# Kernel optimization log

Hardware: AMD Instinct MI355X
Metric: run time of the kernel (lower is better)

Reference implementation:

```python
import jax, jax.numpy as jnp
import numpy as np

LN_EPS = 1e-5


def setup_inputs() -> dict:
    key = jax.random.key(0)
    ks = jax.random.split(key, 10)
    B, T, S, C = 8, 1024, 2048, 1024
    sd = 1.0 / np.sqrt(C)
    return {
        "x": jax.random.normal(ks[0], (B, T, C), jnp.float32),
        "lfb_feats": jax.random.normal(ks[1], (B, S, C), jnp.float32),
        "theta_w": jax.random.normal(ks[2], (C, C), jnp.float32) * sd,
        "theta_b": jax.random.normal(ks[3], (C,), jnp.float32) * 0.01,
        "phi_w": jax.random.normal(ks[4], (C, C), jnp.float32) * sd,
        "phi_b": jax.random.normal(ks[5], (C,), jnp.float32) * 0.01,
        "gi_w": jax.random.normal(ks[6], (C, C), jnp.float32) * sd,
        "gi_b": jax.random.normal(ks[7], (C,), jnp.float32) * 0.01,
        "ln_g": jnp.ones((C,), jnp.float32),
        "ln_b": jnp.zeros((C,), jnp.float32),
        "fc_w": jax.random.normal(ks[8], (C, C), jnp.float32) * sd,
        "fc_b": jax.random.normal(ks[9], (C,), jnp.float32) * 0.01,
    }


def _layernorm(h, g, b):
    mu = jnp.mean(h, axis=-1, keepdims=True)
    var = jnp.var(h, axis=-1, keepdims=True)
    return (h - mu) * jax.lax.rsqrt(var + LN_EPS) * g + b


def reference(x, lfb_feats, theta_w, theta_b, phi_w, phi_b, gi_w, gi_b,
              ln_g, ln_b, fc_w, fc_b):
    # x: [B,T,C], lfb_feats: [B,S,C]. 1x1 Conv1d == per-token linear on channels.
    C = x.shape[-1]
    scale = jnp.sqrt(jnp.asarray(C, x.dtype))  # NOTE: 1/sqrt(1/C) = sqrt(C) (as in source)
    theta = jnp.einsum('btc,oc->bto', x, theta_w) + theta_b          # [B,T,C]
    phi = jnp.einsum('bsc,oc->bso', lfb_feats, phi_w) + phi_b        # [B,S,C]
    gi = jnp.einsum('bsc,oc->bso', lfb_feats, gi_w) + gi_b           # [B,S,C]
    attn = jax.nn.softmax(jnp.einsum('btc,bsc->bts', theta, phi) * scale, axis=-1)
    out = jnp.einsum('bts,bsc->btc', attn, gi)                       # [B,T,C]
    out = jax.nn.relu(_layernorm(out, ln_g, ln_b))
    out = jnp.einsum('btc,oc->bto', out, fc_w) + fc_b                # fc (dropout = identity at eval)
    return out + x                                                   # residual, [B,T,C]
```

## Files before the change

### kernel.cpp

```cpp
#include <hip/hip_runtime.h>


#define BM 128
#define BN 128
#define BK 64

typedef __attribute__((ext_vector_type(8))) short short8;
typedef __attribute__((ext_vector_type(4))) float f32x4;
typedef __attribute__((ext_vector_type(4))) unsigned short us4;

enum { MODE_SPLIT = 0, MODE_TRANS = 1, MODE_F32 = 2, MODE_FINAL = 3 };

__device__ __forceinline__ float b2f(unsigned short u) {
  union { unsigned int i; float f; } x;
  x.i = ((unsigned int)u) << 16;
  return x.f;
}
__device__ __forceinline__ unsigned short f2b(float f) {
  unsigned int u = __float_as_uint(f);
  unsigned int r = (u + 0x7FFFu + ((u >> 16) & 1u)) >> 16;
  return (unsigned short)r;
}

__device__ __forceinline__ void async_cp16(const unsigned short* g,
                                           unsigned short* l) {
  __builtin_amdgcn_global_load_lds(
      (const __attribute__((address_space(1))) void*)g,
      (__attribute__((address_space(3))) void*)l, 16, 0, 0);
}

__global__ __launch_bounds__(256) void split_xlfb(
    const float* __restrict__ lfb, const float* __restrict__ x,
    const float* __restrict__ g, unsigned short* __restrict__ ls,
    unsigned short* __restrict__ xs, float* __restrict__ v, int Ms) {
  const int id = blockIdx.x;
  const int t = threadIdx.x;
  const int c = t * 4;
  if (id < Ms) {
    __shared__ float red[4];
    f32x4 xv = *(const f32x4*)&lfb[(size_t)id * 1024 + c];
    f32x4 gg = *(const f32x4*)&g[c];
    us4 hi, lo;
    float s = 0.f;
#pragma unroll
    for (int i = 0; i < 4; ++i) {
      hi[i] = f2b(xv[i]);
      lo[i] = f2b(xv[i] - b2f(hi[i]));
      s += xv[i] * gg[i];
    }
    *(us4*)&ls[(size_t)id * 2048 + c] = hi;
    *(us4*)&ls[(size_t)id * 2048 + 1024 + c] = lo;
    for (int o = 32; o; o >>= 1) s += __shfl_xor(s, o, 64);
    if ((t & 63) == 0) red[t >> 6] = s;
    __syncthreads();
    if (t == 0) v[id] = red[0] + red[1] + red[2] + red[3];
  } else {
    const int r = id - Ms;
    f32x4 xv = *(const f32x4*)&x[(size_t)r * 1024 + c];
    us4 hi, lo;
#pragma unroll
    for (int i = 0; i < 4; ++i) {
      hi[i] = f2b(xv[i]);
      lo[i] = f2b(xv[i] - b2f(hi[i]));
    }
    *(us4*)&xs[(size_t)r * 2048 + c] = hi;
    *(us4*)&xs[(size_t)r * 2048 + 1024 + c] = lo;
  }
}

__global__ __launch_bounds__(256) void cvt2_bf16(const float* __restrict__ s0,
                                                 unsigned short* __restrict__ d0,
                                                 const float* __restrict__ s1,
                                                 unsigned short* __restrict__ d1) {
  int b = blockIdx.x;
  const float* src = (b < 1024) ? s0 : s1;
  unsigned short* dst = (b < 1024) ? d0 : d1;
  int g = (b & 1023) * 256 + threadIdx.x;
  f32x4 v = *(const f32x4*)&src[g * 4];
  us4 o;
#pragma unroll
  for (int i = 0; i < 4; ++i) o[i] = f2b(v[i]);
  *(us4*)&dst[(size_t)g * 4] = o;
}

__global__ __launch_bounds__(256) void transpose_split2(
    const float* __restrict__ W0, unsigned short* __restrict__ T0,
    const float* __restrict__ W1, unsigned short* __restrict__ T1) {
  __shared__ float tile[64][65];
  const int sel = blockIdx.y >> 4;
  const float* W = sel ? W1 : W0;
  unsigned short* T = sel ? T1 : T0;
  const int bo = (blockIdx.y & 15) * 64;
  const int bc = blockIdx.x * 64;
  const int t = threadIdx.x;
  const int tr = t >> 4;
  const int tc = (t & 15) * 4;
#pragma unroll
  for (int i = 0; i < 4; ++i) {
    f32x4 v = *(const f32x4*)&W[(size_t)(bo + tr + 16 * i) * 1024 + bc + tc];
#pragma unroll
    for (int j = 0; j < 4; ++j) tile[tr + 16 * i][tc + j] = v[j];
  }
  __syncthreads();
#pragma unroll
  for (int i = 0; i < 4; ++i) {
    const int c = bc + tr + 16 * i;
    us4 hi, lo;
#pragma unroll
    for (int j = 0; j < 4; ++j) {
      float v = tile[tc + j][tr + 16 * i];
      hi[j] = f2b(v);
      lo[j] = f2b(v - b2f(hi[j]));
    }
    *(us4*)&T[(size_t)c * 2048 + bo + tc] = hi;
    *(us4*)&T[(size_t)c * 2048 + 1024 + bo + tc] = lo;
  }
}

__global__ __launch_bounds__(256) void make_g(
    const unsigned short* __restrict__ tB, const float* __restrict__ bth,
    float* __restrict__ g) {
  const int d = blockIdx.x * 4 + (threadIdx.x >> 6);
  const int lane = threadIdx.x & 63;
  float s = 0.f;
#pragma unroll
  for (int i = 0; i < 4; ++i) {
    const int o0 = lane * 4 + i * 256;
    us4 h = *(const us4*)&tB[(size_t)d * 2048 + o0];
    us4 lo = *(const us4*)&tB[(size_t)d * 2048 + 1024 + o0];
    f32x4 bb = *(const f32x4*)&bth[o0];
#pragma unroll
    for (int j = 0; j < 4; ++j) s += (b2f(h[j]) + b2f(lo[j])) * bb[j];
  }
  for (int o = 32; o; o >>= 1) s += __shfl_xor(s, o, 64);
  if (lane == 0) g[d] = s;
}

__global__ __launch_bounds__(256) void reduce_g(const float* __restrict__ P,
                                                unsigned short* __restrict__ Gs) {
  const int d = blockIdx.x;
  const int c = threadIdx.x * 4;
  f32x4 s = *(const f32x4*)&P[(size_t)d * 1024 + c];
#pragma unroll
  for (int z = 1; z < 8; ++z) {
    f32x4 p = *(const f32x4*)&P[(size_t)z * 1048576 + (size_t)d * 1024 + c];
#pragma unroll
    for (int i = 0; i < 4; ++i) s[i] += p[i];
  }
  us4 hi, lo;
#pragma unroll
  for (int i = 0; i < 4; ++i) {
    hi[i] = f2b(s[i]);
    lo[i] = f2b(s[i] - b2f(hi[i]));
  }
  *(us4*)&Gs[(size_t)d * 2048 + c] = hi;
  *(us4*)&Gs[(size_t)d * 2048 + 1024 + c] = lo;
}

template <int MODE>
__global__ __launch_bounds__(256, 4) void gemm_bt(
    const unsigned short* __restrict__ A, const unsigned short* __restrict__ B,
    void* __restrict__ Cout, const float* __restrict__ bias,
    const float* __restrict__ resid, int M, int N, int K, int lda, int ldb,
    int ldc, long long sA, long long sB, long long sC, long long sBias,
    int awrap, int awoff, int bwrap, int bwoff, int NBk, int MBk, int mbx,
    int swz, int kzoff) {
  __shared__ __align__(16) unsigned short As[BM * BK];
  __shared__ __align__(16) unsigned short Bs[BN * BK];

  const int tid = threadIdx.x;
  const int l = tid & 63;
  const int w = tid >> 6;
  const int wm = w >> 1, wn = w & 1;
  const int ln = l & 15, lq = l >> 4;

  int bmi, bni, bzi;
  {
    const int id = blockIdx.x;
    if (swz == 1) {
      bzi = id & 7;
      const int r = id >> 3;
      bmi = r % mbx;
      bni = r / mbx;
    } else if (swz == 2) {
      bzi = 0;
      const int r = id >> 3;
      bmi = (id & 7) * mbx + r % mbx;
      bni = r / mbx;
    } else {
      bni = id % NBk;
      const int rem = id / NBk;
      bmi = rem % MBk;
      bzi = rem / MBk;
    }
  }
  const int bm = bmi * BM;
  const int bn = bni * BN;
  const unsigned short* Ab = A + (size_t)bzi * (size_t)sA;
  const unsigned short* Bb = B + (size_t)bzi * (size_t)sB;
  const float* bz = bias ? bias + (size_t)bzi * (size_t)sBias : nullptr;
  const int kbase = bzi * kzoff;

  const int arow = tid >> 3;
  const int acol = (((tid & 7) ^ ((tid >> 3) & 7)) * 8);
  const int ldsbase = (tid & 0xC0) * 8;

  f32x4 acc[4][4];
#pragma unroll
  for (int i = 0; i < 4; ++i)
#pragma unroll
    for (int j = 0; j < 4; ++j) acc[i][j] = (f32x4){0.f, 0.f, 0.f, 0.f};

  const int sw = ln & 7;

  for (int k0 = 0; k0 < K; k0 += BK) {
    const int kg = k0 + kbase;
    const int ka = (kg < awrap) ? kg : kg - awoff;
    const int kb = (kg < bwrap) ? kg : kg - bwoff;
#pragma unroll
    for (int it = 0; it < 4; ++it) {
      const int r = it * 32 + arow;
      async_cp16(Ab + (size_t)(bm + r) * lda + ka + acol,
                 &As[it * 2048 + ldsbase]);
    }
#pragma unroll
    for (int it = 0; it < 4; ++it) {
      const int r = it * 32 + arow;
      async_cp16(Bb + (size_t)(bn + r) * ldb + kb + acol,
                 &Bs[it * 2048 + ldsbase]);
    }
    __syncthreads();

#pragma unroll
    for (int ks = 0; ks < 2; ++ks) {
      short8 a[4], b[4];
      const int kof = ((ks * 4 + lq) ^ sw) * 8;
#pragma unroll
      for (int i = 0; i < 4; ++i)
        a[i] = *(const short8*)&As[(wm * 64 + i * 16 + ln) * BK + kof];
#pragma unroll
      for (int j = 0; j < 4; ++j)
        b[j] = *(const short8*)&Bs[(wn * 64 + j * 16 + ln) * BK + kof];
#pragma unroll
      for (int i = 0; i < 4; ++i)
#pragma unroll
        for (int j = 0; j < 4; ++j)
          acc[i][j] = __builtin_amdgcn_mfma_f32_16x16x32_bf16(a[i], b[j],
                                                              acc[i][j], 0, 0, 0);
    }
    __syncthreads();
  }

  float* Cf = (float*)Cout + (size_t)bzi * (size_t)sC;
  unsigned short* Cb = (unsigned short*)Cout + (size_t)bzi * (size_t)sC;

  if constexpr (MODE == MODE_TRANS) {
#pragma unroll
    for (int i = 0; i < 4; ++i) {
      const int gm0 = bm + wm * 64 + i * 16 + lq * 4;
      const int bt = gm0 >> 11;
      const int sr = gm0 & 2047;
#pragma unroll
      for (int j = 0; j < 4; ++j) {
        const int gn = bn + wn * 64 + j * 16 + ln;
        const float bv2 = (bz != nullptr) ? bz[gn] : 0.f;
        us4 o;
#pragma unroll
        for (int r = 0; r < 4; ++r) o[r] = f2b(acc[i][j][r] + bv2);
        *(us4*)&Cb[(size_t)bt * 2097152 + (size_t)gn * 2048 + sr] = o;
      }
    }
  } else {
#pragma unroll
    for (int j = 0; j < 4; ++j) {
      const int gn = bn + wn * 64 + j * 16 + ln;
      const float bv2 = (bz != nullptr) ? bz[gn] : 0.f;
#pragma unroll
      for (int i = 0; i < 4; ++i) {
        const int gm0 = bm + wm * 64 + i * 16 + lq * 4;
#pragma unroll
        for (int r = 0; r < 4; ++r) {
          const int gm = gm0 + r;
          const float v = acc[i][j][r] + bv2;
          if constexpr (MODE == MODE_SPLIT) {
            unsigned short hi = f2b(v);
            Cb[(size_t)gm * ldc + gn] = hi;
            Cb[(size_t)gm * ldc + gn + (ldc >> 1)] = f2b(v - b2f(hi));
          } else if constexpr (MODE == MODE_F32) {
            Cf[(size_t)gm * ldc + gn] = v;
          } else if constexpr (MODE == MODE_FINAL) {
            const size_t idx = (size_t)gm * ldc + gn;
            Cf[idx] = v + resid[idx];
          }
        }
      }
    }
  }
}

__global__ __launch_bounds__(256) void softmax_rows(
    const float* __restrict__ logit, unsigned short* __restrict__ attn) {
  const int row = blockIdx.x;
  const float* L = logit + (size_t)row * 2048;
  unsigned short* O = attn + (size_t)row * 2048;
  const int t = threadIdx.x;
  __shared__ float red[8];

  f32x4 v0 = *(const f32x4*)&L[t * 4];
  f32x4 v1 = *(const f32x4*)&L[t * 4 + 1024];
  float m = fmaxf(fmaxf(fmaxf(v0[0], v0[1]), fmaxf(v0[2], v0[3])),
                  fmaxf(fmaxf(v1[0], v1[1]), fmaxf(v1[2], v1[3])));
  for (int o = 32; o; o >>= 1) m = fmaxf(m, __shfl_xor(m, o, 64));
  if ((t & 63) == 0) red[t >> 6] = m;
  __syncthreads();
  m = fmaxf(fmaxf(red[0], red[1]), fmaxf(red[2], red[3]));

  float e[8];
  float s = 0.f;
#pragma unroll
  for (int i = 0; i < 4; ++i) { e[i] = __expf(32.f * (v0[i] - m)); s += e[i]; }
#pragma unroll
  for (int i = 0; i < 4; ++i) { e[4 + i] = __expf(32.f * (v1[i] - m)); s += e[4 + i]; }
  for (int o = 32; o; o >>= 1) s += __shfl_xor(s, o, 64);
  if ((t & 63) == 0) red[4 + (t >> 6)] = s;
  __syncthreads();
  s = red[4] + red[5] + red[6] + red[7];
  const float inv = 1.f / s;
  us4 o0, o1;
#pragma unroll
  for (int i = 0; i < 4; ++i) { o0[i] = f2b(e[i] * inv); o1[i] = f2b(e[4 + i] * inv); }
  *(us4*)&O[t * 4] = o0;
  *(us4*)&O[t * 4 + 1024] = o1;
}

__global__ __launch_bounds__(256) void ln_relu(
    const float* __restrict__ X, const float* __restrict__ g,
    const float* __restrict__ b, unsigned short* __restrict__ H) {
  const int row = blockIdx.x;
  const float* x = X + (size_t)row * 1024;
  unsigned short* h = H + (size_t)row * 1024;
  const int t = threadIdx.x;
  __shared__ float red[8];
  f32x4 v = *(const f32x4*)&x[t * 4];
  float s = v[0] + v[1] + v[2] + v[3];
  float q = v[0] * v[0] + v[1] * v[1] + v[2] * v[2] + v[3] * v[3];
  for (int o = 32; o; o >>= 1) {
    s += __shfl_xor(s, o, 64);
    q += __shfl_xor(q, o, 64);
  }
  if ((t & 63) == 0) { red[t >> 6] = s; red[4 + (t >> 6)] = q; }
  __syncthreads();
  s = red[0] + red[1] + red[2] + red[3];
  q = red[4] + red[5] + red[6] + red[7];
  const float mean = s * (1.f / 1024.f);
  const float var = q * (1.f / 1024.f) - mean * mean;
  const float rstd = rsqrtf(var + 1e-5f);
  us4 o;
#pragma unroll
  for (int i = 0; i < 4; ++i) {
    const int c = t * 4 + i;
    const float y = (v[i] - mean) * rstd * g[c] + b[c];
    o[i] = f2b(fmaxf(y, 0.f));
  }
  *(us4*)&h[t * 4] = o;
}

extern "C" void kernel_launch(void* const* d_in, const int* in_sizes, int n_in,
                              void* d_out, int out_size, void* d_ws,
                              size_t ws_size, hipStream_t stream) {
  const float* x = (const float*)d_in[0];
  const float* lfb = (const float*)d_in[1];
  const float* th_w = (const float*)d_in[2];
  const float* th_b = (const float*)d_in[3];
  const float* ph_w = (const float*)d_in[4];
  const float* gi_w = (const float*)d_in[6];
  const float* gi_b = (const float*)d_in[7];
  const float* lng = (const float*)d_in[8];
  const float* lnb = (const float*)d_in[9];
  const float* fc_w = (const float*)d_in[10];
  const float* fc_b = (const float*)d_in[11];
  float* outf = (float*)d_out;
  char* ws = (char*)d_ws;

  const size_t MB = 1048576;
  int nb = 1;
  for (int cand = 8; cand >= 1; cand >>= 1)
    if ((size_t)cand * 24 * MB + 18 * MB <= ws_size) { nb = cand; break; }

  char* tail = ws + (size_t)nb * 24 * MB;
  unsigned short* tA = (unsigned short*)(tail);
  unsigned short* tB = (unsigned short*)(tail + 4 * MB);
  unsigned short* Gs = (unsigned short*)(tail + 8 * MB);
  unsigned short* giw = (unsigned short*)(tail + 12 * MB);
  unsigned short* fcw = (unsigned short*)(tail + 14 * MB);
  float* gv = (float*)(tail + 16 * MB);
  float* vb = (float*)(tail + 16 * MB + 65536);

  dim3 blk(256);
  transpose_split2<<<dim3(16, 32), blk, 0, stream>>>(th_w, tA, ph_w, tB);
  make_g<<<dim3(256), blk, 0, stream>>>(tB, th_b, gv);
  if (nb >= 2) {
    float* gpart = (float*)ws;
    gemm_bt<MODE_F32><<<dim3(512), blk, 0, stream>>>(
        tB, tA, gpart, nullptr, nullptr, 1024, 1024, 384, 2048, 2048, 1024,
        0, 0, 1048576LL, 0, 2048, 2048, 1024, 1024, 8, 8, 8, 1, 384);
    reduce_g<<<dim3(1024), blk, 0, stream>>>(gpart, Gs);
  } else {
    gemm_bt<MODE_SPLIT><<<dim3(64), blk, 0, stream>>>(
        tB, tA, Gs, nullptr, nullptr, 1024, 1024, 3072, 2048, 2048, 2048,
        0, 0, 0, 0, 2048, 2048, 1024, 1024, 8, 8, 1, 2, 0);
  }
  cvt2_bf16<<<dim3(2048), blk, 0, stream>>>(gi_w, giw, fc_w, fcw);

  for (int b0 = 0; b0 < 8; b0 += nb) {
    unsigned short* xs = (unsigned short*)(ws);
    float* logit = (float*)(ws);
    unsigned short* ls = (unsigned short*)(ws + (size_t)nb * 8 * MB);
    unsigned short* ys = (unsigned short*)(ws + (size_t)nb * 16 * MB);
    unsigned short* giT = (unsigned short*)(ws + (size_t)nb * 20 * MB);
    unsigned short* attn = ys;
    float* outp = (float*)ws;
    unsigned short* h = giT;

    const float* xb = x + (size_t)b0 * 1048576;
    const float* lfbb = lfb + (size_t)b0 * 2097152;
    float* ob = outf + (size_t)b0 * 1048576;
    const int Ms = nb * 2048;
    const int Mt = nb * 1024;
    const int zswz = (nb == 8) ? 1 : 0;

    split_xlfb<<<dim3(Ms + Mt), blk, 0, stream>>>(lfbb, xb, gv, ls, xs, vb, Ms);
    gemm_bt<MODE_TRANS><<<dim3(8 * (Ms / 128)), blk, 0, stream>>>(
        ls, giw, giT, gi_b, nullptr, Ms, 1024, 1024, 2048, 1024, 2048,
        0, 0, 0, 0, 1024, 0, 1024, 0, 8, Ms / 128, Ms / 1024, 2, 0);
    gemm_bt<MODE_SPLIT><<<dim3(8 * (Mt / 128)), blk, 0, stream>>>(
        xs, Gs, ys, nullptr, nullptr, Mt, 1024, 3072, 2048, 2048, 2048,
        0, 0, 0, 0, 2048, 2048, 1024, 1024, 8, Mt / 128, Mt / 1024, 2, 0);
    gemm_bt<MODE_F32><<<dim3(16 * 8 * nb), blk, 0, stream>>>(
        ys, ls, logit, vb, nullptr, 1024, 2048, 3072, 2048, 2048, 2048,
        2097152LL, 4194304LL, 2097152LL, 2048LL, 2048, 2048, 1024, 1024,
        16, 8, 8, zswz, 0);
    softmax_rows<<<dim3(Mt), blk, 0, stream>>>(logit, attn);
    gemm_bt<MODE_F32><<<dim3(8 * 8 * nb), blk, 0, stream>>>(
        attn, giT, outp, nullptr, nullptr, 1024, 1024, 2048, 2048, 2048, 1024,
        2097152LL, 2097152LL, 1048576LL, 0, 2048, 0, 2048, 0, 8, 8, 8, zswz, 0);
    ln_relu<<<dim3(Mt), blk, 0, stream>>>(outp, lng, lnb, h);
    gemm_bt<MODE_FINAL><<<dim3(8 * (Mt / 128)), blk, 0, stream>>>(
        h, fcw, ob, fc_b, xb, Mt, 1024, 1024, 1024, 1024, 1024,
        0, 0, 0, 0, 1024, 0, 1024, 0, 8, Mt / 128, Mt / 1024, 2, 0);
  }
}
```

Measured before the change: 514.2 us.

## Add 256x256-tile 8-wave GEMM kernel for gi projection and logits GEMMs

Result: faster. 501.3 us (-2.5%).

```diff
diff --git a/kernel.cpp b/kernel.cpp
--- a/kernel.cpp
+++ b/kernel.cpp
@@ -298,6 +298,203 @@
   }
 }
 
+__device__ __forceinline__ void ld8f(const unsigned short* Lb, int roff, int ln,
+                                     int lq, int sw, short8* a) {
+#pragma unroll
+  for (int mi = 0; mi < 4; ++mi)
+#pragma unroll
+    for (int ks = 0; ks < 2; ++ks)
+      a[mi * 2 + ks] = *(const short8*)&Lb[(roff + mi * 16 + ln) * 64 +
+                                           (((ks * 4 + lq) ^ sw) * 8)];
+}
+__device__ __forceinline__ void ld4f(const unsigned short* Lb, int roff, int ln,
+                                     int lq, int sw, short8* b) {
+#pragma unroll
+  for (int ni = 0; ni < 2; ++ni)
+#pragma unroll
+    for (int ks = 0; ks < 2; ++ks)
+      b[ni * 2 + ks] = *(const short8*)&Lb[(roff + ni * 16 + ln) * 64 +
+                                           (((ks * 4 + lq) ^ sw) * 8)];
+}
+template <int MH, int NH>
+__device__ __forceinline__ void mfmaQ(f32x4 (&acc)[8][4], const short8* a,
+                                      const short8* b) {
+  __builtin_amdgcn_s_setprio(1);
+#pragma unroll
+  for (int mi = 0; mi < 4; ++mi)
+#pragma unroll
+    for (int ni = 0; ni < 2; ++ni)
+#pragma unroll
+      for (int ks = 0; ks < 2; ++ks)
+        acc[MH * 4 + mi][NH * 2 + ni] = __builtin_amdgcn_mfma_f32_16x16x32_bf16(
+            a[mi * 2 + ks], b[ni * 2 + ks], acc[MH * 4 + mi][NH * 2 + ni], 0, 0,
+            0);
+  __builtin_amdgcn_s_setprio(0);
+}
+
+template <int MODE>
+__global__ __launch_bounds__(512, 1) void gemm8(
+    const unsigned short* __restrict__ A, const unsigned short* __restrict__ B,
+    void* __restrict__ Cout, const float* __restrict__ bias, int M, int N,
+    int K, int lda, int ldb, int ldc, long long sA, long long sB, long long sC,
+    long long sBias, int awrap, int awoff, int bwrap, int bwoff, int NBk,
+    int MBk, int mbx, int swz) {
+  __shared__ __align__(16) unsigned short lds[2][4][8192];
+
+  const int tid = threadIdx.x;
+  const int l = tid & 63;
+  const int w = tid >> 6;
+  const int wm = w >> 2;
+  const int wn = w & 3;
+  const int ln = l & 15, lq = l >> 4;
+  const int sw = ln & 7;
+
+  int bmi, bni, bzi;
+  {
+    const int id = blockIdx.x;
+    if (swz == 1) {
+      bzi = id & 7;
+      const int r = id >> 3;
+      bmi = r % mbx;
+      bni = r / mbx;
+    } else if (swz == 2) {
+      bzi = 0;
+      const int r = id >> 3;
+      bmi = (id & 7) * mbx + r % mbx;
+      bni = r / mbx;
+    } else {
+      bni = id % NBk;
+      const int rem = id / NBk;
+      bmi = rem % MBk;
+      bzi = rem / MBk;
+    }
+  }
+  const int bm = bmi * 256;
+  const int bn = bni * 256;
+  const unsigned short* Ab = A + (size_t)bzi * (size_t)sA;
+  const unsigned short* Bb = B + (size_t)bzi * (size_t)sB;
+  const float* bz = bias ? bias + (size_t)bzi * (size_t)sBias : nullptr;
+
+  const int srow = tid >> 3;
+  const int schk = ((tid & 7) ^ ((tid >> 3) & 7)) * 8;
+  const int sdst0 = (tid & 448) * 8;
+
+  auto stageA = [&](int d, int half, int kk) {
+#pragma unroll
+    for (int j = 0; j < 2; ++j)
+      async_cp16(Ab + (size_t)(bm + half * 128 + srow + j * 64) * lda + kk +
+                     schk,
+                 &lds[d][half][sdst0 + j * 4096]);
+  };
+  auto stageB = [&](int d, int half, int kk) {
+#pragma unroll
+    for (int j = 0; j < 2; ++j)
+      async_cp16(Bb + (size_t)(bn + half * 128 + srow + j * 64) * ldb + kk +
+                     schk,
+                 &lds[d][2 + half][sdst0 + j * 4096]);
+  };
+  auto wrapA = [&](int kg) { return (kg < awrap) ? kg : kg - awoff; };
+  auto wrapB = [&](int kg) { return (kg < bwrap) ? kg : kg - bwoff; };
+
+  f32x4 acc[8][4];
+#pragma unroll
+  for (int i = 0; i < 8; ++i)
+#pragma unroll
+    for (int j = 0; j < 4; ++j) acc[i][j] = (f32x4){0.f, 0.f, 0.f, 0.f};
+
+  const int nt = K >> 6;
+
+  stageA(0, 0, wrapA(0));
+  stageA(0, 1, wrapA(0));
+  stageB(0, 0, wrapB(0));
+  stageB(0, 1, wrapB(0));
+  if (nt > 1) {
+    stageB(1, 0, wrapB(64));
+    stageB(1, 1, wrapB(64));
+    asm volatile("s_waitcnt vmcnt(4)" : : : "memory");
+  } else {
+    asm volatile("s_waitcnt vmcnt(0)" : : : "memory");
+  }
+  __builtin_amdgcn_s_barrier();
+
+  const unsigned short* LA;
+  const unsigned short* LB;
+  short8 a0[8], a1[8], b0[4], b1[4];
+  const int broff = (wn & 1) * 64;
+  const int bslot = 2 + (wn >> 1);
+
+  for (int t = 0; t < nt; ++t) {
+    const int d = t & 1;
+    LA = &lds[d][wm][0];
+    LB = &lds[d][bslot][0];
+    ld8f(LA, 0, ln, lq, sw, a0);
+    ld4f(LB, broff, ln, lq, sw, b0);
+    if (t + 1 < nt) stageA(d ^ 1, 0, wrapA((t + 1) * 64));
+    __builtin_amdgcn_s_barrier();
+    asm volatile("s_waitcnt lgkmcnt(0)" : : : "memory");
+    __builtin_amdgcn_sched_barrier(0);
+    mfmaQ<0, 0>(acc, a0, b0);
+    __builtin_amdgcn_s_barrier();
+    ld4f(LB, broff + 32, ln, lq, sw, b1);
+    if (t + 1 < nt) stageA(d ^ 1, 1, wrapA((t + 1) * 64));
+    __builtin_amdgcn_s_barrier();
+    asm volatile("s_waitcnt lgkmcnt(0)" : : : "memory");
+    __builtin_amdgcn_sched_barrier(0);
+    mfmaQ<0, 1>(acc, a0, b1);
+    __builtin_amdgcn_s_barrier();
+    ld8f(LA, 64, ln, lq, sw, a1);
+    if (t + 2 < nt) stageB(d, 0, wrapB((t + 2) * 64));
+    __builtin_amdgcn_s_barrier();
+    asm volatile("s_waitcnt lgkmcnt(0)" : : : "memory");
+    __builtin_amdgcn_sched_barrier(0);
+    mfmaQ<1, 1>(acc, a1, b1);
+    __builtin_amdgcn_s_barrier();
+    if (t + 2 < nt) stageB(d, 1, wrapB((t + 2) * 64));
+    __builtin_amdgcn_s_barrier();
+    mfmaQ<1, 0>(acc, a1, b0);
+    if (t + 2 < nt) {
+      asm volatile("s_waitcnt vmcnt(4)" : : : "memory");
+    } else {
+      asm volatile("s_waitcnt vmcnt(0)" : : : "memory");
+    }
+    __builtin_amdgcn_s_barrier();
+  }
+
+  float* Cf = (float*)Cout + (size_t)bzi * (size_t)sC;
+  unsigned short* Cb = (unsigned short*)Cout;
+
+  if constexpr (MODE == MODE_TRANS) {
+#pragma unroll
+    for (int mi = 0; mi < 8; ++mi) {
+      const int gm0 = bm + wm * 128 + mi * 16 + lq * 4;
+      const int bt = gm0 >> 11;
+      const int sr = gm0 & 2047;
+#pragma unroll
+      for (int ni = 0; ni < 4; ++ni) {
+        const int gn = bn + wn * 64 + ni * 16 + ln;
+        const float bv2 = (bz != nullptr) ? bz[gn] : 0.f;
+        us4 o;
+#pragma unroll
+        for (int r = 0; r < 4; ++r) o[r] = f2b(acc[mi][ni][r] + bv2);
+        *(us4*)&Cb[(size_t)bt * 2097152 + (size_t)gn * 2048 + sr] = o;
+      }
+    }
+  } else {
+#pragma unroll
+    for (int ni = 0; ni < 4; ++ni) {
+      const int gn = bn + wn * 64 + ni * 16 + ln;
+      const float bv2 = (bz != nullptr) ? bz[gn] : 0.f;
+#pragma unroll
+      for (int mi = 0; mi < 8; ++mi) {
+        const int gm0 = bm + wm * 128 + mi * 16 + lq * 4;
+#pragma unroll
+        for (int r = 0; r < 4; ++r)
+          Cf[(size_t)(gm0 + r) * ldc + gn] = acc[mi][ni][r] + bv2;
+      }
+    }
+  }
+}
+
 __global__ __launch_bounds__(256) void softmax_rows(
     const float* __restrict__ logit, unsigned short* __restrict__ attn) {
   const int row = blockIdx.x;
@@ -430,16 +627,16 @@
     const int zswz = (nb == 8) ? 1 : 0;
 
     split_xlfb<<<dim3(Ms + Mt), blk, 0, stream>>>(lfbb, xb, gv, ls, xs, vb, Ms);
-    gemm_bt<MODE_TRANS><<<dim3(8 * (Ms / 128)), blk, 0, stream>>>(
-        ls, giw, giT, gi_b, nullptr, Ms, 1024, 1024, 2048, 1024, 2048,
-        0, 0, 0, 0, 1024, 0, 1024, 0, 8, Ms / 128, Ms / 1024, 2, 0);
+    gemm8<MODE_TRANS><<<dim3(32 * nb), dim3(512), 0, stream>>>(
+        ls, giw, giT, gi_b, Ms, 1024, 1024, 2048, 1024, 2048,
+        0LL, 0LL, 0LL, 0LL, 1024, 0, 1024, 0, 4, 8 * nb, nb, 2);
     gemm_bt<MODE_SPLIT><<<dim3(8 * (Mt / 128)), blk, 0, stream>>>(
         xs, Gs, ys, nullptr, nullptr, Mt, 1024, 3072, 2048, 2048, 2048,
         0, 0, 0, 0, 2048, 2048, 1024, 1024, 8, Mt / 128, Mt / 1024, 2, 0);
-    gemm_bt<MODE_F32><<<dim3(16 * 8 * nb), blk, 0, stream>>>(
-        ys, ls, logit, vb, nullptr, 1024, 2048, 3072, 2048, 2048, 2048,
+    gemm8<MODE_F32><<<dim3(32 * nb), dim3(512), 0, stream>>>(
+        ys, ls, logit, vb, 1024, 2048, 3072, 2048, 2048, 2048,
         2097152LL, 4194304LL, 2097152LL, 2048LL, 2048, 2048, 1024, 1024,
-        16, 8, 8, zswz, 0);
+        8, 4, 4, zswz);
     softmax_rows<<<dim3(Mt), blk, 0, stream>>>(logit, attn);
     gemm_bt<MODE_F32><<<dim3(8 * 8 * nb), blk, 0, stream>>>(
         attn, giT, outp, nullptr, nullptr, 1024, 1024, 2048, 2048, 2048, 1024,
```
